# Optimization experiments

Measured on AMD Instinct MI355X. Metric: run time of the kernel, lower is better.

Reference implementation:

```python
import jax, jax.numpy as jnp
import numpy as np

N = 16384      # nodes
E = 131072     # edges
L = 256        # latent size
H = 256        # mlp hidden size
S = 4          # message passing steps
OUT = 128      # decoder node output size
EPS = 1e-6     # flax LayerNorm epsilon


def _mlp(x, W0, b0, W1, b1):
    h = jax.nn.relu(x @ W0 + b0)
    return h @ W1 + b1


def _mlp_ln(x, W0, b0, W1, b1, ls, lb):
    y = _mlp(x, W0, b0, W1, b1)
    mu = y.mean(-1, keepdims=True)
    var = ((y - mu) ** 2).mean(-1, keepdims=True)
    return (y - mu) * jax.lax.rsqrt(var + EPS) * ls + lb


def setup_inputs() -> dict:
    key = jax.random.key(0)
    ks = iter(jax.random.split(key, 64))
    std = 0.02

    def w(shape):
        return jax.random.normal(next(ks), shape, dtype=jnp.float32) * std

    inp = {
        'node_feats': jax.random.normal(next(ks), (N, 3), dtype=jnp.float32),
        'edge_feats': jax.random.normal(next(ks), (E, 4), dtype=jnp.float32),
        'senders': jax.random.randint(next(ks), (E,), 0, N, dtype=jnp.int32),
        'receivers': jax.random.randint(next(ks), (E,), 0, N, dtype=jnp.int32),
        # node embedder MLP (3 -> H -> L) + LayerNorm
        'en_W0': w((3, H)), 'en_b0': jnp.zeros((H,)), 'en_W1': w((H, L)), 'en_b1': jnp.zeros((L,)),
        'en_ls': jnp.ones((L,)), 'en_lb': jnp.zeros((L,)),
        # edge embedder MLP (4 -> H -> L) + LayerNorm
        'ee_W0': w((4, H)), 'ee_b0': jnp.zeros((H,)), 'ee_W1': w((H, L)), 'ee_b1': jnp.zeros((L,)),
        'ee_ls': jnp.ones((L,)), 'ee_lb': jnp.zeros((L,)),
        # processor edge MLPs, stacked over S steps (3L -> H -> L) + LN
        'pe_W0': w((S, 3 * L, H)), 'pe_b0': jnp.zeros((S, H)), 'pe_W1': w((S, H, L)), 'pe_b1': jnp.zeros((S, L)),
        'pe_ls': jnp.ones((S, L)), 'pe_lb': jnp.zeros((S, L)),
        # processor node MLPs, stacked over S steps (2L -> H -> L) + LN
        'pn_W0': w((S, 2 * L, H)), 'pn_b0': jnp.zeros((S, H)), 'pn_W1': w((S, H, L)), 'pn_b1': jnp.zeros((S, L)),
        'pn_ls': jnp.ones((S, L)), 'pn_lb': jnp.zeros((S, L)),
        # node decoder MLP (L -> H -> OUT), no LayerNorm
        'dn_W0': w((L, H)), 'dn_b0': jnp.zeros((H,)), 'dn_W1': w((H, OUT)), 'dn_b1': jnp.zeros((OUT,)),
    }
    return inp


def reference(node_feats, edge_feats, senders, receivers,
              en_W0, en_b0, en_W1, en_b1, en_ls, en_lb,
              ee_W0, ee_b0, ee_W1, ee_b1, ee_ls, ee_lb,
              pe_W0, pe_b0, pe_W1, pe_b1, pe_ls, pe_lb,
              pn_W0, pn_b0, pn_W1, pn_b1, pn_ls, pn_lb,
              dn_W0, dn_b0, dn_W1, dn_b1):
    # Embed raw node/edge features into latent space.
    nodes = _mlp_ln(node_feats, en_W0, en_b0, en_W1, en_b1, en_ls, en_lb)   # [N, L]
    edges = _mlp_ln(edge_feats, ee_W0, ee_b0, ee_W1, ee_b1, ee_ls, ee_lb)   # [E, L]

    def step(carry, p):
        nodes, edges = carry
        (eW0, eb0, eW1, eb1, els, elb, nW0, nb0, nW1, nb1, nls, nlb) = p
        # Edge update: MLP on [edge, sender_node, receiver_node].
        ein = jnp.concatenate([edges, nodes[senders], nodes[receivers]], axis=-1)  # [E, 3L]
        new_e = _mlp_ln(ein, eW0, eb0, eW1, eb1, els, elb)                          # [E, L]
        # Aggregate new edge messages into receiver nodes (segment_sum).
        agg = jax.ops.segment_sum(new_e, receivers, num_segments=N)                # [N, L]
        # Node update: MLP on [node, aggregated messages].
        nin = jnp.concatenate([nodes, agg], axis=-1)                                # [N, 2L]
        new_n = _mlp_ln(nin, nW0, nb0, nW1, nb1, nls, nlb)                          # [N, L]
        # Residual connections (as in DeepTypedGraphNet processor).
        return (nodes + new_n, edges + new_e), None

    (nodes, edges), _ = jax.lax.scan(
        step, (nodes, edges),
        (pe_W0, pe_b0, pe_W1, pe_b1, pe_ls, pe_lb,
         pn_W0, pn_b0, pn_W1, pn_b1, pn_ls, pn_lb))

    # Decoder on nodes (no LayerNorm on the output head).
    out = _mlp(nodes, dn_W0, dn_b0, dn_W1, dn_b1)  # [N, OUT]
    return out
```

## Files before the change

kernel.cpp:

```cpp
#include <hip/hip_runtime.h>
#include <hip/hip_bf16.h>

#define NN 16384
#define NE 131072
#define L 256
#define SSTEPS 4
#define OUTD 128

typedef __attribute__((ext_vector_type(8))) short bf16x8;
typedef __attribute__((ext_vector_type(4))) float f32x4;

typedef const unsigned __attribute__((address_space(1)))* as1_u32p;
typedef unsigned __attribute__((address_space(3)))* as3_u32p;

__device__ __forceinline__ void gload16(const void* g, void* lds) {
  __builtin_amdgcn_global_load_lds((as1_u32p)g, (as3_u32p)lds, 16, 0, 0);
}

__device__ __forceinline__ short f2bs(float f) {
  unsigned u = __builtin_bit_cast(unsigned, f);
  u = (u + 0x7fffu + ((u >> 16) & 1u)) >> 16;
  return (short)u;
}
__device__ __forceinline__ float bs2f(short s) {
  unsigned u = ((unsigned)(unsigned short)s) << 16;
  return __builtin_bit_cast(float, u);
}
__device__ __forceinline__ unsigned cvt_pk_bf16(float lo, float hi) {
  unsigned r;
  asm("v_cvt_pk_bf16_f32 %0, %1, %2" : "=v"(r) : "v"(lo), "v"(hi));
  return r;
}
__device__ __forceinline__ bf16x8 pack_bf16x8(const float v[8]) {
  union { unsigned u[4]; bf16x8 b; } r;
#pragma unroll
  for (int k = 0; k < 4; ++k) r.u[k] = cvt_pk_bf16(v[2 * k], v[2 * k + 1]);
  return r.b;
}

__device__ __forceinline__ void store_tile(short* hs, int l, int mi, int nb,
                                           f32x4 v) {
  const int lm = l & 15, g = l >> 4;
#pragma unroll
  for (int i = 0; i < 4; ++i) {
    const float part = __shfl_xor(v[i], 1);
    if ((l & 1) == 0) {
      const int row = mi * 16 + g * 4 + i;
      const int col = nb + lm;
      const int off = (row * 512 + col * 2) ^ ((row & 7) << 4);
      *(unsigned*)((char*)hs + off) = cvt_pk_bf16(v[i], part);
    }
  }
}

template <int MI, int NT, int KC, int AST>
__device__ __forceinline__ void gemm_lds(const short* __restrict__ Wp,
                                         int Ncols, const short* hs, int n0,
                                         int l, f32x4 acc[MI][NT]) {
  const int lm = l & 15, g = l >> 4;
#pragma unroll
  for (int kc = 0; kc < KC; ++kc) {
    bf16x8 a[MI];
#pragma unroll
    for (int mi = 0; mi < MI; ++mi) {
      const int row = mi * 16 + lm;
      const int off = (row * AST + kc * 64 + g * 16) ^ ((row & 7) << 4);
      a[mi] = *(const bf16x8*)((const char*)hs + off);
    }
#pragma unroll
    for (int ni = 0; ni < NT; ++ni) {
      const int n = n0 + ni * 16 + lm;
      bf16x8 b = *(const bf16x8*)(Wp + ((size_t)kc * Ncols + n) * 32 + g * 8);
#pragma unroll
      for (int mi = 0; mi < MI; ++mi)
        acc[mi][ni] =
            __builtin_amdgcn_mfma_f32_16x16x32_bf16(a[mi], b, acc[mi][ni], 0, 0, 0);
    }
  }
}

__global__ void pack_w(const float* __restrict__ src, short* __restrict__ dst,
                       int K, int N, int cnt) {
  const size_t total = (size_t)K * N * cnt;
  for (size_t i = (size_t)blockIdx.x * blockDim.x + threadIdx.x; i < total;
       i += (size_t)gridDim.x * blockDim.x) {
    const size_t mat = i / ((size_t)K * N);
    const int rem = (int)(i - mat * (size_t)K * N);
    const int k = rem / N, n = rem - k * N;
    dst[mat * (size_t)K * N + ((size_t)(k >> 5) * N + n) * 32 + (k & 31)] =
        f2bs(src[i]);
  }
}

__global__ void pack_w0_pad(const float* __restrict__ src,
                            short* __restrict__ dst, int Kreal) {
  const int i = blockIdx.x * 256 + threadIdx.x;
  if (i >= 256 * 32) return;
  const int n = i >> 5, k = i & 31;
  dst[n * 32 + k] = (k < Kreal) ? f2bs(src[k * 256 + n]) : (short)0;
}

__device__ __forceinline__ void stage_tile256(const short* __restrict__ src0,
                                              short* As, int w, int l) {
#pragma unroll
  for (int i = 0; i < 4; ++i) {
    const int rbase = w * 8 + i * 2;
    const int r = rbase + (l >> 5);
    const int boff = ((l & 31) * 16) ^ ((r & 7) << 4);
    gload16((const char*)(src0 + (size_t)r * L) + boff, As + rbase * 256);
  }
}

__device__ __forceinline__ void stage_tile512(const short* __restrict__ a_src,
                                              const short* __restrict__ b_src,
                                              short* As, int w, int l, int n0) {
#pragma unroll
  for (int i = 0; i < 8; ++i) {
    const int r = w * 8 + i;
    const int cb = (l * 16) ^ ((r & 7) << 4);
    const int cs = cb >> 1;
    const short* src = (cs < 256)
                           ? a_src + (size_t)(n0 + r) * L + cs
                           : b_src + (size_t)(n0 + r) * L + (cs - 256);
    gload16(src, As + r * 512);
  }
}

__global__ void csr_hist(const int* __restrict__ recv, int* __restrict__ deg) {
  const int e = blockIdx.x * 256 + threadIdx.x;
  atomicAdd(&deg[recv[e]], 1);
}
__global__ __launch_bounds__(256) void csr_scan(const int* __restrict__ deg,
                                                int* __restrict__ start,
                                                int* __restrict__ cursor) {
  __shared__ int part[256];
  const int t = threadIdx.x;
  int s = 0;
  for (int i = 0; i < NN / 256; ++i) s += deg[t * (NN / 256) + i];
  part[t] = s;
  __syncthreads();
  if (t == 0) {
    int acc = 0;
    for (int i = 0; i < 256; ++i) {
      const int v = part[i];
      part[i] = acc;
      acc += v;
    }
  }
  __syncthreads();
  int acc = part[t];
  for (int i = 0; i < NN / 256; ++i) {
    const int n = t * (NN / 256) + i;
    start[n] = acc;
    cursor[n] = acc;
    acc += deg[n];
  }
  if (t == 255) start[NN] = acc;
}
__global__ void csr_scatter(const int* __restrict__ recv,
                            int* __restrict__ cursor, int* __restrict__ elist) {
  const int e = blockIdx.x * 256 + threadIdx.x;
  const int p = atomicAdd(&cursor[recv[e]], 1);
  elist[p] = e;
}
__global__ void csr_sort(const int* __restrict__ start, int* __restrict__ elist) {
  const int n = blockIdx.x * blockDim.x + threadIdx.x;
  if (n >= NN) return;
  const int b = start[n], e = start[n + 1];
  for (int i = b + 1; i < e; ++i) {
    const int v = elist[i];
    int j = i - 1;
    while (j >= b && elist[j] > v) {
      elist[j + 1] = elist[j];
      --j;
    }
    elist[j + 1] = v;
  }
}

__global__ __launch_bounds__(256) void agg_gather(
    const short* __restrict__ new_e, const int* __restrict__ start,
    const int* __restrict__ elist, short* __restrict__ agg_b) {
  const int t = threadIdx.x, w = t >> 6, l = t & 63;
  const int half = l >> 5, lc = l & 31;
  const int n = blockIdx.x * 8 + w * 2 + half;
  const int b = start[n], e = start[n + 1];
  float acc[8] = {0.f, 0.f, 0.f, 0.f, 0.f, 0.f, 0.f, 0.f};
#pragma unroll 2
  for (int j = b; j < e; ++j) {
    const int eid = elist[j];
    const bf16x8 v = *(const bf16x8*)(new_e + (size_t)eid * L + lc * 8);
#pragma unroll
    for (int k = 0; k < 8; ++k) acc[k] += bs2f(v[k]);
  }
  *(bf16x8*)(agg_b + (size_t)n * L + lc * 8) = pack_bf16x8(acc);
}

__device__ __forceinline__ void ln_row(const short* smem, int row, int seg,
                                       const float lsv[16], const float lbv[16],
                                       float ne[16]) {
  const int off0 = (row * 512 + seg * 16) ^ ((row & 7) << 4);
  const int off1 = (row * 512 + 256 + seg * 16) ^ ((row & 7) << 4);
  const bf16x8 y0 = *(const bf16x8*)((const char*)smem + off0);
  const bf16x8 y1 = *(const bf16x8*)((const char*)smem + off1);
  float v[16];
#pragma unroll
  for (int k = 0; k < 8; ++k) {
    v[k] = bs2f(y0[k]);
    v[8 + k] = bs2f(y1[k]);
  }
  float s = 0.f;
#pragma unroll
  for (int k = 0; k < 16; ++k) s += v[k];
#pragma unroll
  for (int o = 1; o < 16; o <<= 1) s += __shfl_xor(s, o);
  const float mu = s * (1.f / 256.f);
  float sq = 0.f;
#pragma unroll
  for (int k = 0; k < 16; ++k) {
    const float d = v[k] - mu;
    sq += d * d;
  }
#pragma unroll
  for (int o = 1; o < 16; o <<= 1) sq += __shfl_xor(sq, o);
  const float rstd = rsqrtf(sq * (1.f / 256.f) + 1e-6f);
#pragma unroll
  for (int k = 0; k < 16; ++k) ne[k] = (v[k] - mu) * rstd * lsv[k] + lbv[k];
}

__device__ __forceinline__ void load16(const float* __restrict__ p, int seg,
                                       float d[16]) {
  const float4 a0 = *(const float4*)(p + seg * 8);
  const float4 a1 = *(const float4*)(p + seg * 8 + 4);
  const float4 a2 = *(const float4*)(p + 128 + seg * 8);
  const float4 a3 = *(const float4*)(p + 128 + seg * 8 + 4);
  d[0] = a0.x; d[1] = a0.y; d[2] = a0.z; d[3] = a0.w;
  d[4] = a1.x; d[5] = a1.y; d[6] = a1.z; d[7] = a1.w;
  d[8] = a2.x; d[9] = a2.y; d[10] = a2.z; d[11] = a2.w;
  d[12] = a3.x; d[13] = a3.y; d[14] = a3.z; d[15] = a3.w;
}

__global__ __launch_bounds__(256, 4) void proj_mfma(
    const short* __restrict__ nodes_b, const short* __restrict__ Wfull,
    short* __restrict__ NSb, short* __restrict__ NRb) {
  __shared__ char smem[16384];
  short* As = (short*)smem;
  const int t = threadIdx.x, w = t >> 6, l = t & 63;
  const int tr = t >> 4, seg = t & 15;
  const int n0 = blockIdx.x * 32;
  const short* Wp = Wfull + (size_t)(8 + blockIdx.y * 8) * 256 * 32;
  short* out = blockIdx.y ? NRb : NSb;

  stage_tile256(nodes_b + (size_t)n0 * L, As, w, l);
  __syncthreads();

  f32x4 acc[2][4] = {};
  gemm_lds<2, 4, 8, 512>(Wp, L, As, w * 64, l, acc);
  __syncthreads();
#pragma unroll
  for (int ni = 0; ni < 4; ++ni)
#pragma unroll
    for (int mi = 0; mi < 2; ++mi)
      store_tile(As, l, mi, w * 64 + ni * 16, acc[mi][ni]);
  __syncthreads();

#pragma unroll
  for (int p = 0; p < 2; ++p) {
    const int row = p * 16 + tr;
    const int off0 = (row * 512 + seg * 16) ^ ((row & 7) << 4);
    const int off1 = (row * 512 + 256 + seg * 16) ^ ((row & 7) << 4);
    *(bf16x8*)(out + (size_t)(n0 + row) * L + seg * 8) =
        *(const bf16x8*)((const char*)As + off0);
    *(bf16x8*)(out + (size_t)(n0 + row) * L + 128 + seg * 8) =
        *(const bf16x8*)((const char*)As + off1);
  }
}

__global__ __launch_bounds__(256, 4) void edge_step_mfma(
    const short* __restrict__ NSb, const short* __restrict__ NRb,
    short* __restrict__ edges_b, short* __restrict__ new_e,
    const int* __restrict__ senders, const int* __restrict__ receivers,
    const short* __restrict__ W0p, const float* __restrict__ b0,
    const short* __restrict__ W1p, const float* __restrict__ b1,
    const float* __restrict__ ls, const float* __restrict__ lb) {
  __shared__ char smem[32768];
  short* As = (short*)smem;
  short* nsrB = (short*)(smem + 16384);
  const int t = threadIdx.x, w = t >> 6, l = t & 63;
  const int lm = l & 15, g = l >> 4;
  const int tr = t >> 4, seg = t & 15;
  const int e0 = blockIdx.x * 32;

  const int sn0 = senders[e0 + tr], rc0 = receivers[e0 + tr];
  const int sn1 = senders[e0 + 16 + tr], rc1 = receivers[e0 + 16 + tr];
  stage_tile256(edges_b + (size_t)e0 * L, As, w, l);
  __syncthreads();

  bf16x8 gn[2][2], gr[2][2];
  {
    const short* p0 = NSb + (size_t)sn0 * L + seg * 8;
    gn[0][0] = *(const bf16x8*)p0;
    gn[0][1] = *(const bf16x8*)(p0 + 128);
    const short* p1 = NSb + (size_t)sn1 * L + seg * 8;
    gn[1][0] = *(const bf16x8*)p1;
    gn[1][1] = *(const bf16x8*)(p1 + 128);
    const short* q0 = NRb + (size_t)rc0 * L + seg * 8;
    gr[0][0] = *(const bf16x8*)q0;
    gr[0][1] = *(const bf16x8*)(q0 + 128);
    const short* q1 = NRb + (size_t)rc1 * L + seg * 8;
    gr[1][0] = *(const bf16x8*)q1;
    gr[1][1] = *(const bf16x8*)(q1 + 128);
  }

  f32x4 acc[2][4] = {};
  gemm_lds<2, 4, 8, 512>(W0p, L, As, w * 64, l, acc);

  bf16x8 old0[2], old1[2];
#pragma unroll
  for (int p = 0; p < 2; ++p) {
    const int row = p * 16 + tr;
    old0[p] = *(const bf16x8*)((const char*)As +
                               ((row * 512 + seg * 16) ^ ((row & 7) << 4)));
    old1[p] = *(const bf16x8*)((const char*)As +
                               ((row * 512 + 256 + seg * 16) ^ ((row & 7) << 4)));
  }

#pragma unroll
  for (int p = 0; p < 2; ++p) {
    const int row = p * 16 + tr;
    float s[16];
#pragma unroll
    for (int k = 0; k < 8; ++k) {
      s[k] = bs2f(gn[p][0][k]) + bs2f(gr[p][0][k]);
      s[8 + k] = bs2f(gn[p][1][k]) + bs2f(gr[p][1][k]);
    }
    const int off0 = (row * 512 + seg * 16) ^ ((row & 7) << 4);
    const int off1 = (row * 512 + 256 + seg * 16) ^ ((row & 7) << 4);
    *(bf16x8*)((char*)nsrB + off0) = pack_bf16x8(s);
    *(bf16x8*)((char*)nsrB + off1) = pack_bf16x8(s + 8);
  }
  __syncthreads();

#pragma unroll
  for (int ni = 0; ni < 4; ++ni) {
    const float bia = b0[w * 64 + ni * 16 + lm];
    const int col = w * 64 + ni * 16 + lm;
#pragma unroll
    for (int mi = 0; mi < 2; ++mi) {
      f32x4 v = acc[mi][ni];
#pragma unroll
      for (int i = 0; i < 4; ++i) {
        const int row = mi * 16 + g * 4 + i;
        const int noff = (row * 512 + col * 2) ^ ((row & 7) << 4);
        v[i] = fmaxf(v[i] + bia + bs2f(*(const short*)((const char*)nsrB + noff)),
                     0.f);
      }
      store_tile(As, l, mi, w * 64 + ni * 16, v);
    }
  }
  __syncthreads();

  f32x4 acc2[2][4] = {};
  gemm_lds<2, 4, 8, 512>(W1p, L, As, w * 64, l, acc2);
#pragma unroll
  for (int ni = 0; ni < 4; ++ni) {
    const float bia = b1[w * 64 + ni * 16 + lm];
#pragma unroll
    for (int mi = 0; mi < 2; ++mi) {
      f32x4 v = acc2[mi][ni];
#pragma unroll
      for (int i = 0; i < 4; ++i) v[i] += bia;
      store_tile(nsrB, l, mi, w * 64 + ni * 16, v);
    }
  }
  __syncthreads();

  float lsv[16], lbv[16];
  load16(ls, seg, lsv);
  load16(lb, seg, lbv);
#pragma unroll
  for (int p = 0; p < 2; ++p) {
    const int row = p * 16 + tr;
    float ne[16];
    ln_row(nsrB, row, seg, lsv, lbv, ne);
    const size_t e = (size_t)(e0 + row);
    *(bf16x8*)(new_e + e * L + seg * 8) = pack_bf16x8(ne);
    *(bf16x8*)(new_e + e * L + 128 + seg * 8) = pack_bf16x8(ne + 8);
    float r0[8], r1[8];
#pragma unroll
    for (int k = 0; k < 8; ++k) {
      r0[k] = bs2f(old0[p][k]) + ne[k];
      r1[k] = bs2f(old1[p][k]) + ne[8 + k];
    }
    *(bf16x8*)(edges_b + e * L + seg * 8) = pack_bf16x8(r0);
    *(bf16x8*)(edges_b + e * L + 128 + seg * 8) = pack_bf16x8(r1);
  }
}

__global__ __launch_bounds__(256, 4) void node_step_mfma(
    float* __restrict__ nodes_f, short* __restrict__ nodes_b,
    const short* __restrict__ agg_b, const short* __restrict__ W0p,
    const float* __restrict__ b0, const short* __restrict__ W1p,
    const float* __restrict__ b1, const float* __restrict__ ls,
    const float* __restrict__ lb, const short* __restrict__ W0nS,
    const short* __restrict__ W0nR, short* __restrict__ NSb,
    short* __restrict__ NRb) {
  __shared__ char smem[32768];
  short* As = (short*)smem;
  short* hb = (short*)smem;
  short* yb = (short*)(smem + 16384);
  const int t = threadIdx.x, w = t >> 6, l = t & 63;
  const int lm = l & 15;
  const int tr = t >> 4, seg = t & 15;
  const int n0 = blockIdx.x * 32;

  stage_tile512(nodes_b, agg_b, As, w, l, n0);
  __syncthreads();

  f32x4 acc[2][4] = {};
  gemm_lds<2, 4, 16, 1024>(W0p, L, As, w * 64, l, acc);
  __syncthreads();

#pragma unroll
  for (int ni = 0; ni < 4; ++ni) {
    const float bia = b0[w * 64 + ni * 16 + lm];
#pragma unroll
    for (int mi = 0; mi < 2; ++mi) {
      f32x4 v = acc[mi][ni];
#pragma unroll
      for (int i = 0; i < 4; ++i) v[i] = fmaxf(v[i] + bia, 0.f);
      store_tile(hb, l, mi, w * 64 + ni * 16, v);
    }
  }
  __syncthreads();

  f32x4 acc2[2][4] = {};
  gemm_lds<2, 4, 8, 512>(W1p, L, hb, w * 64, l, acc2);
  __syncthreads();
#pragma unroll
  for (int ni = 0; ni < 4; ++ni) {
    const float bia = b1[w * 64 + ni * 16 + lm];
#pragma unroll
    for (int mi = 0; mi < 2; ++mi) {
      f32x4 v = acc2[mi][ni];
#pragma unroll
      for (int i = 0; i < 4; ++i) v[i] += bia;
      store_tile(yb, l, mi, w * 64 + ni * 16, v);
    }
  }
  __syncthreads();

  float lsv[16], lbv[16];
  load16(ls, seg, lsv);
  load16(lb, seg, lbv);
#pragma unroll
  for (int p = 0; p < 2; ++p) {
    const int row = p * 16 + tr;
    float ne[16];
    ln_row(yb, row, seg, lsv, lbv, ne);
    const size_t n = (size_t)(n0 + row);
    float* nf = nodes_f + n * L;
    float fv[16];
    load16(nf, seg, fv);
    float nv[16];
#pragma unroll
    for (int k = 0; k < 16; ++k) nv[k] = fv[k] + ne[k];
    *(float4*)(nf + seg * 8) = make_float4(nv[0], nv[1], nv[2], nv[3]);
    *(float4*)(nf + seg * 8 + 4) = make_float4(nv[4], nv[5], nv[6], nv[7]);
    *(float4*)(nf + 128 + seg * 8) = make_float4(nv[8], nv[9], nv[10], nv[11]);
    *(float4*)(nf + 128 + seg * 8 + 4) = make_float4(nv[12], nv[13], nv[14], nv[15]);
    const bf16x8 nb0 = pack_bf16x8(nv);
    const bf16x8 nb1 = pack_bf16x8(nv + 8);
    *(bf16x8*)(nodes_b + n * L + seg * 8) = nb0;
    *(bf16x8*)(nodes_b + n * L + 128 + seg * 8) = nb1;
    const int off0 = (row * 512 + seg * 16) ^ ((row & 7) << 4);
    const int off1 = (row * 512 + 256 + seg * 16) ^ ((row & 7) << 4);
    *(bf16x8*)((char*)hb + off0) = nb0;
    *(bf16x8*)((char*)hb + off1) = nb1;
  }

  if (W0nS == nullptr) return;
  __syncthreads();

  {
    f32x4 pa[2][4] = {};
    gemm_lds<2, 4, 8, 512>(W0nS, L, hb, w * 64, l, pa);
#pragma unroll
    for (int ni = 0; ni < 4; ++ni)
#pragma unroll
      for (int mi = 0; mi < 2; ++mi)
        store_tile(yb, l, mi, w * 64 + ni * 16, pa[mi][ni]);
    __syncthreads();
#pragma unroll
    for (int p = 0; p < 2; ++p) {
      const int row = p * 16 + tr;
      const int off0 = (row * 512 + seg * 16) ^ ((row & 7) << 4);
      const int off1 = (row * 512 + 256 + seg * 16) ^ ((row & 7) << 4);
      *(bf16x8*)(NSb + (size_t)(n0 + row) * L + seg * 8) =
          *(const bf16x8*)((const char*)yb + off0);
      *(bf16x8*)(NSb + (size_t)(n0 + row) * L + 128 + seg * 8) =
          *(const bf16x8*)((const char*)yb + off1);
    }
  }
  __syncthreads();

  {
    f32x4 pa[2][4] = {};
    gemm_lds<2, 4, 8, 512>(W0nR, L, hb, w * 64, l, pa);
#pragma unroll
    for (int ni = 0; ni < 4; ++ni)
#pragma unroll
      for (int mi = 0; mi < 2; ++mi)
        store_tile(yb, l, mi, w * 64 + ni * 16, pa[mi][ni]);
    __syncthreads();
#pragma unroll
    for (int p = 0; p < 2; ++p) {
      const int row = p * 16 + tr;
      const int off0 = (row * 512 + seg * 16) ^ ((row & 7) << 4);
      const int off1 = (row * 512 + 256 + seg * 16) ^ ((row & 7) << 4);
      *(bf16x8*)(NRb + (size_t)(n0 + row) * L + seg * 8) =
          *(const bf16x8*)((const char*)yb + off0);
      *(bf16x8*)(NRb + (size_t)(n0 + row) * L + 128 + seg * 8) =
          *(const bf16x8*)((const char*)yb + off1);
    }
  }
}

template <int K1, bool WF32>
__global__ __launch_bounds__(256) void embed_mfma(
    const float* __restrict__ x, const short* __restrict__ W0p,
    const float* __restrict__ b0, const short* __restrict__ W1p,
    const float* __restrict__ b1, const float* __restrict__ ls,
    const float* __restrict__ lb, float* __restrict__ dst_f,
    short* __restrict__ dst_b) {
  __shared__ short hs[64 * 256];
  __shared__ short xsb[64 * 32];
  const int t = threadIdx.x, w = t >> 6, l = t & 63;
  const int lm = l & 15, g = l >> 4;
  const int tr = t >> 4, seg = t & 15;
  const int r0 = blockIdx.x * 64;

  if (t < 64) {
    const float* xr = x + (size_t)(r0 + t) * K1;
    float v[8] = {0.f, 0.f, 0.f, 0.f, 0.f, 0.f, 0.f, 0.f};
#pragma unroll
    for (int k = 0; k < K1; ++k) v[k] = xr[k];
    bf16x8 z;
#pragma unroll
    for (int k = 0; k < 8; ++k) z[k] = 0;
    char* rb = (char*)xsb + t * 64;
    *(bf16x8*)(rb + (0 ^ ((t & 3) << 4))) = pack_bf16x8(v);
#pragma unroll
    for (int gi = 1; gi < 4; ++gi) *(bf16x8*)(rb + ((gi * 16) ^ ((t & 3) << 4))) = z;
  }
  __syncthreads();

  f32x4 acc[4][4] = {};
  {
    bf16x8 a[4];
#pragma unroll
    for (int mi = 0; mi < 4; ++mi) {
      const int row = mi * 16 + lm;
      a[mi] = *(const bf16x8*)((const char*)xsb + row * 64 +
                               ((g * 16) ^ ((row & 3) << 4)));
    }
#pragma unroll
    for (int ni = 0; ni < 4; ++ni) {
      const int n = w * 64 + ni * 16 + lm;
      bf16x8 b = *(const bf16x8*)(W0p + n * 32 + g * 8);
#pragma unroll
      for (int mi = 0; mi < 4; ++mi)
        acc[mi][ni] =
            __builtin_amdgcn_mfma_f32_16x16x32_bf16(a[mi], b, acc[mi][ni], 0, 0, 0);
    }
  }
#pragma unroll
  for (int ni = 0; ni < 4; ++ni) {
    const float bia = b0[w * 64 + ni * 16 + lm];
#pragma unroll
    for (int mi = 0; mi < 4; ++mi) {
      f32x4 v = acc[mi][ni];
#pragma unroll
      for (int i = 0; i < 4; ++i) v[i] = fmaxf(v[i] + bia, 0.f);
      store_tile(hs, l, mi, w * 64 + ni * 16, v);
    }
  }
  __syncthreads();

  f32x4 acc2[4][4] = {};
  gemm_lds<4, 4, 8, 512>(W1p, L, hs, w * 64, l, acc2);
  __syncthreads();
#pragma unroll
  for (int ni = 0; ni < 4; ++ni) {
    const float bia = b1[w * 64 + ni * 16 + lm];
#pragma unroll
    for (int mi = 0; mi < 4; ++mi) {
      f32x4 v = acc2[mi][ni];
#pragma unroll
      for (int i = 0; i < 4; ++i) v[i] += bia;
      store_tile(hs, l, mi, w * 64 + ni * 16, v);
    }
  }
  __syncthreads();

  float lsv[16], lbv[16];
  load16(ls, seg, lsv);
  load16(lb, seg, lbv);
#pragma unroll
  for (int p = 0; p < 4; ++p) {
    const int row = p * 16 + tr;
    float ne[16];
    ln_row(hs, row, seg, lsv, lbv, ne);
    const size_t n = (size_t)(r0 + row);
    *(bf16x8*)(dst_b + n * L + seg * 8) = pack_bf16x8(ne);
    *(bf16x8*)(dst_b + n * L + 128 + seg * 8) = pack_bf16x8(ne + 8);
    if (WF32) {
      float* df = dst_f + n * L;
      *(float4*)(df + seg * 8) = make_float4(ne[0], ne[1], ne[2], ne[3]);
      *(float4*)(df + seg * 8 + 4) = make_float4(ne[4], ne[5], ne[6], ne[7]);
      *(float4*)(df + 128 + seg * 8) = make_float4(ne[8], ne[9], ne[10], ne[11]);
      *(float4*)(df + 128 + seg * 8 + 4) =
          make_float4(ne[12], ne[13], ne[14], ne[15]);
    }
  }
}

__global__ __launch_bounds__(256) void decoder_mfma(
    const short* __restrict__ nodes_b, const short* __restrict__ W0p,
    const float* __restrict__ b0, const short* __restrict__ W1p,
    const float* __restrict__ b1, float* __restrict__ out) {
  __shared__ short hs[64 * 256];
  const int t = threadIdx.x, w = t >> 6, l = t & 63;
  const int lm = l & 15, g = l >> 4;
  const int n0 = blockIdx.x * 64;

  const short* baseA[4];
#pragma unroll
  for (int mi = 0; mi < 4; ++mi)
    baseA[mi] = nodes_b + (size_t)(n0 + mi * 16 + lm) * L;

  f32x4 acc[4][4] = {};
#pragma unroll
  for (int kc = 0; kc < 8; ++kc) {
    const int koff = kc * 32 + g * 8;
    bf16x8 a[4];
#pragma unroll
    for (int mi = 0; mi < 4; ++mi) a[mi] = *(const bf16x8*)(baseA[mi] + koff);
#pragma unroll
    for (int ni = 0; ni < 4; ++ni) {
      const int n = w * 64 + ni * 16 + lm;
      bf16x8 b = *(const bf16x8*)(W0p + ((size_t)kc * L + n) * 32 + g * 8);
#pragma unroll
      for (int mi = 0; mi < 4; ++mi)
        acc[mi][ni] = __builtin_amdgcn_mfma_f32_16x16x32_bf16(a[mi], b,
                                                             acc[mi][ni],
                                                             0, 0, 0);
    }
  }
#pragma unroll
  for (int ni = 0; ni < 4; ++ni) {
    const float bia = b0[w * 64 + ni * 16 + lm];
#pragma unroll
    for (int mi = 0; mi < 4; ++mi) {
      f32x4 v = acc[mi][ni];
#pragma unroll
      for (int i = 0; i < 4; ++i) v[i] = fmaxf(v[i] + bia, 0.f);
      store_tile(hs, l, mi, w * 64 + ni * 16, v);
    }
  }
  __syncthreads();

  f32x4 acc2[4][2] = {};
  gemm_lds<4, 2, 8, 512>(W1p, OUTD, hs, w * 32, l, acc2);

  float b14[2];
#pragma unroll
  for (int ni = 0; ni < 2; ++ni) b14[ni] = b1[w * 32 + ni * 16 + lm];
#pragma unroll
  for (int mi = 0; mi < 4; ++mi)
#pragma unroll
    for (int ni = 0; ni < 2; ++ni)
#pragma unroll
      for (int i = 0; i < 4; ++i) {
        const int row = n0 + mi * 16 + g * 4 + i;
        const int col = w * 32 + ni * 16 + lm;
        out[(size_t)row * OUTD + col] = acc2[mi][ni][i] + b14[ni];
      }
}

extern "C" void kernel_launch(void* const* d_in, const int* in_sizes, int n_in,
                              void* d_out, int out_size, void* d_ws,
                              size_t ws_size, hipStream_t stream) {
  const float* node_feats = (const float*)d_in[0];
  const float* edge_feats = (const float*)d_in[1];
  const int* senders = (const int*)d_in[2];
  const int* receivers = (const int*)d_in[3];
  auto f = [&](int i) { return (const float*)d_in[i]; };

  char* p = (char*)d_ws;
  auto alloc = [&](size_t bytes) {
    char* q = p;
    p += (bytes + 255) & ~(size_t)255;
    return q;
  };
  float* nodes_f = (float*)alloc((size_t)NN * L * 4);
  short* nodes_b = (short*)alloc((size_t)NN * L * 2);
  short* edges_b = (short*)alloc((size_t)NE * L * 2);
  short* new_e = (short*)alloc((size_t)NE * L * 2);
  short* agg_b = (short*)alloc((size_t)NN * L * 2);
  short* NSb = (short*)alloc((size_t)NN * L * 2);
  short* NRb = (short*)alloc((size_t)NN * L * 2);
  int* deg = (int*)alloc((size_t)NN * 4);
  int* start = (int*)alloc((size_t)(NN + 16) * 4);
  int* cursor = (int*)alloc((size_t)NN * 4);
  int* elist = (int*)alloc((size_t)NE * 4);
  short* en_W0p = (short*)alloc(256 * 32 * 2);
  short* ee_W0p = (short*)alloc(256 * 32 * 2);
  short* en_W1p = (short*)alloc(65536 * 2);
  short* ee_W1p = (short*)alloc(65536 * 2);
  short* pe_W0p = (short*)alloc((size_t)4 * 768 * 256 * 2);
  short* pe_W1p = (short*)alloc((size_t)4 * 65536 * 2);
  short* pn_W0p = (short*)alloc((size_t)4 * 512 * 256 * 2);
  short* pn_W1p = (short*)alloc((size_t)4 * 65536 * 2);
  short* dn_W0p = (short*)alloc(65536 * 2);
  short* dn_W1p = (short*)alloc(32768 * 2);

  hipMemsetAsync(deg, 0, (size_t)NN * 4, stream);
  csr_hist<<<NE / 256, 256, 0, stream>>>(receivers, deg);
  csr_scan<<<1, 256, 0, stream>>>(deg, start, cursor);
  csr_scatter<<<NE / 256, 256, 0, stream>>>(receivers, cursor, elist);
  csr_sort<<<NN / 256, 256, 0, stream>>>(start, elist);

  pack_w0_pad<<<32, 256, 0, stream>>>(f(4), en_W0p, 3);
  pack_w0_pad<<<32, 256, 0, stream>>>(f(10), ee_W0p, 4);
  pack_w<<<256, 256, 0, stream>>>(f(6), en_W1p, 256, 256, 1);
  pack_w<<<256, 256, 0, stream>>>(f(12), ee_W1p, 256, 256, 1);
  pack_w<<<1024, 256, 0, stream>>>(f(16), pe_W0p, 768, 256, 4);
  pack_w<<<512, 256, 0, stream>>>(f(18), pe_W1p, 256, 256, 4);
  pack_w<<<1024, 256, 0, stream>>>(f(22), pn_W0p, 512, 256, 4);
  pack_w<<<512, 256, 0, stream>>>(f(24), pn_W1p, 256, 256, 4);
  pack_w<<<256, 256, 0, stream>>>(f(28), dn_W0p, 256, 256, 1);
  pack_w<<<128, 256, 0, stream>>>(f(30), dn_W1p, 256, 128, 1);

  embed_mfma<3, true><<<NN / 64, 256, 0, stream>>>(
      node_feats, en_W0p, f(5), en_W1p, f(7), f(8), f(9), nodes_f, nodes_b);
  embed_mfma<4, false><<<NE / 64, 256, 0, stream>>>(
      edge_feats, ee_W0p, f(11), ee_W1p, f(13), f(14), f(15), nullptr, edges_b);

  for (int s = 0; s < SSTEPS; ++s) {
    const short* W0s = pe_W0p + (size_t)s * 768 * 256;
    if (s == 0)
      proj_mfma<<<dim3(NN / 32, 2), 256, 0, stream>>>(nodes_b, W0s, NSb, NRb);
    edge_step_mfma<<<NE / 32, 256, 0, stream>>>(
        NSb, NRb, edges_b, new_e, senders, receivers, W0s,
        f(17) + (size_t)s * 256, pe_W1p + (size_t)s * 65536,
        f(19) + (size_t)s * 256, f(20) + (size_t)s * 256,
        f(21) + (size_t)s * 256);
    agg_gather<<<NN / 8, 256, 0, stream>>>(new_e, start, elist, agg_b);
    const short* W0n = (s + 1 < SSTEPS) ? pe_W0p + (size_t)(s + 1) * 768 * 256
                                        : nullptr;
    node_step_mfma<<<NN / 32, 256, 0, stream>>>(
        nodes_f, nodes_b, agg_b, pn_W0p + (size_t)s * 512 * 256,
        f(23) + (size_t)s * 256, pn_W1p + (size_t)s * 65536,
        f(25) + (size_t)s * 256, f(26) + (size_t)s * 256,
        f(27) + (size_t)s * 256, W0n ? W0n + (size_t)8 * 256 * 32 : nullptr,
        W0n ? W0n + (size_t)16 * 256 * 32 : nullptr, NSb, NRb);
  }

  decoder_mfma<<<NN / 64, 256, 0, stream>>>(nodes_b, dn_W0p, f(29), dn_W1p,
                                            f(31), (float*)d_out);
}
```

Baseline: 814.5 us.

## Fuse receiver segment-sum gather into node step kernel and raise edge occupancy

Removes the separate agg_gather kernel. Each node_step block now gathers and sums the incoming edge messages for its 32 nodes directly into the swizzled LDS tile, next to the staged node features. This avoids writing and reading back the aggregated buffer and one launch per step, but the gather now runs with fewer blocks and may leave less latency hiding. The edge kernel's launch bound is also raised to 5 blocks per CU, which may constrain registers.

```diff
diff --git a/kernel.cpp b/kernel.cpp
--- a/kernel.cpp
+++ b/kernel.cpp
@@ -111,18 +111,16 @@
   }
 }
 
-__device__ __forceinline__ void stage_tile512(const short* __restrict__ a_src,
-                                              const short* __restrict__ b_src,
-                                              short* As, int w, int l, int n0) {
+__device__ __forceinline__ void stage_nodes_half(const short* __restrict__ a_src,
+                                                 short* As, int w, int l,
+                                                 int n0) {
 #pragma unroll
   for (int i = 0; i < 8; ++i) {
     const int r = w * 8 + i;
-    const int cb = (l * 16) ^ ((r & 7) << 4);
-    const int cs = cb >> 1;
-    const short* src = (cs < 256)
-                           ? a_src + (size_t)(n0 + r) * L + cs
-                           : b_src + (size_t)(n0 + r) * L + (cs - 256);
-    gload16(src, As + r * 512);
+    if (l < 32) {
+      const int cb = (l * 16) ^ ((r & 7) << 4);
+      gload16((const char*)(a_src + (size_t)(n0 + r) * L) + cb, As + r * 512);
+    }
   }
 }
 
@@ -178,24 +176,6 @@
   }
 }
 
-__global__ __launch_bounds__(256) void agg_gather(
-    const short* __restrict__ new_e, const int* __restrict__ start,
-    const int* __restrict__ elist, short* __restrict__ agg_b) {
-  const int t = threadIdx.x, w = t >> 6, l = t & 63;
-  const int half = l >> 5, lc = l & 31;
-  const int n = blockIdx.x * 8 + w * 2 + half;
-  const int b = start[n], e = start[n + 1];
-  float acc[8] = {0.f, 0.f, 0.f, 0.f, 0.f, 0.f, 0.f, 0.f};
-#pragma unroll 2
-  for (int j = b; j < e; ++j) {
-    const int eid = elist[j];
-    const bf16x8 v = *(const bf16x8*)(new_e + (size_t)eid * L + lc * 8);
-#pragma unroll
-    for (int k = 0; k < 8; ++k) acc[k] += bs2f(v[k]);
-  }
-  *(bf16x8*)(agg_b + (size_t)n * L + lc * 8) = pack_bf16x8(acc);
-}
-
 __device__ __forceinline__ void ln_row(const short* smem, int row, int seg,
                                        const float lsv[16], const float lbv[16],
                                        float ne[16]) {
@@ -276,7 +256,7 @@
   }
 }
 
-__global__ __launch_bounds__(256, 4) void edge_step_mfma(
+__global__ __launch_bounds__(256, 5) void edge_step_mfma(
     const short* __restrict__ NSb, const short* __restrict__ NRb,
     short* __restrict__ edges_b, short* __restrict__ new_e,
     const int* __restrict__ senders, const int* __restrict__ receivers,
@@ -399,7 +379,8 @@
 
 __global__ __launch_bounds__(256, 4) void node_step_mfma(
     float* __restrict__ nodes_f, short* __restrict__ nodes_b,
-    const short* __restrict__ agg_b, const short* __restrict__ W0p,
+    const short* __restrict__ new_e, const int* __restrict__ start,
+    const int* __restrict__ elist, const short* __restrict__ W0p,
     const float* __restrict__ b0, const short* __restrict__ W1p,
     const float* __restrict__ b1, const float* __restrict__ ls,
     const float* __restrict__ lb, const short* __restrict__ W0nS,
@@ -414,7 +395,27 @@
   const int tr = t >> 4, seg = t & 15;
   const int n0 = blockIdx.x * 32;
 
-  stage_tile512(nodes_b, agg_b, As, w, l, n0);
+  stage_nodes_half(nodes_b, As, w, l, n0);
+
+  {
+    const int grp = t >> 5, lc = t & 31;
+#pragma unroll
+    for (int i = 0; i < 4; ++i) {
+      const int r = grp * 4 + i;
+      const int n = n0 + r;
+      const int b = start[n], e = start[n + 1];
+      float acc[8] = {0.f, 0.f, 0.f, 0.f, 0.f, 0.f, 0.f, 0.f};
+#pragma unroll 2
+      for (int j = b; j < e; ++j) {
+        const bf16x8 v =
+            *(const bf16x8*)(new_e + (size_t)elist[j] * L + lc * 8);
+#pragma unroll
+        for (int k = 0; k < 8; ++k) acc[k] += bs2f(v[k]);
+      }
+      const int off = (r * 1024 + 512 + lc * 16) ^ ((r & 7) << 4);
+      *(bf16x8*)((char*)As + off) = pack_bf16x8(acc);
+    }
+  }
   __syncthreads();
 
   f32x4 acc[2][4] = {};
@@ -707,7 +708,6 @@
   short* nodes_b = (short*)alloc((size_t)NN * L * 2);
   short* edges_b = (short*)alloc((size_t)NE * L * 2);
   short* new_e = (short*)alloc((size_t)NE * L * 2);
-  short* agg_b = (short*)alloc((size_t)NN * L * 2);
   short* NSb = (short*)alloc((size_t)NN * L * 2);
   short* NRb = (short*)alloc((size_t)NN * L * 2);
   int* deg = (int*)alloc((size_t)NN * 4);
@@ -756,14 +756,14 @@
         f(17) + (size_t)s * 256, pe_W1p + (size_t)s * 65536,
         f(19) + (size_t)s * 256, f(20) + (size_t)s * 256,
         f(21) + (size_t)s * 256);
-    agg_gather<<<NN / 8, 256, 0, stream>>>(new_e, start, elist, agg_b);
     const short* W0n = (s + 1 < SSTEPS) ? pe_W0p + (size_t)(s + 1) * 768 * 256
                                         : nullptr;
     node_step_mfma<<<NN / 32, 256, 0, stream>>>(
-        nodes_f, nodes_b, agg_b, pn_W0p + (size_t)s * 512 * 256,
-        f(23) + (size_t)s * 256, pn_W1p + (size_t)s * 65536,
-        f(25) + (size_t)s * 256, f(26) + (size_t)s * 256,
-        f(27) + (size_t)s * 256, W0n ? W0n + (size_t)8 * 256 * 32 : nullptr,
+        nodes_f, nodes_b, new_e, start, elist,
+        pn_W0p + (size_t)s * 512 * 256, f(23) + (size_t)s * 256,
+        pn_W1p + (size_t)s * 65536, f(25) + (size_t)s * 256,
+        f(26) + (size_t)s * 256, f(27) + (size_t)s * 256,
+        W0n ? W0n + (size_t)8 * 256 * 32 : nullptr,
         W0n ? W0n + (size_t)16 * 256 * 32 : nullptr, NSb, NRb);
   }
 
```

Measured after the change: 935.5 us. +14.9%, slower.
